# Performance work log

Measured on AMD Instinct MI355X. Metric: run time of the kernel, lower is better.

The kernel has to match this reference:

```python
import jax, jax.numpy as jnp
import numpy as np

EPS = 1e-5
K = 20  # n. neighbors


def _lrelu(x):
    return jnp.where(x >= 0, x, 0.2 * x)


def _bn(x, gamma, beta):
    # training-mode batchnorm over all axes except channel axis 1
    axes = tuple(i for i in range(x.ndim) if i != 1)
    m = jnp.mean(x, axis=axes, keepdims=True)
    v = jnp.var(x, axis=axes, keepdims=True)
    shape = [1, x.shape[1]] + [1] * (x.ndim - 2)
    return (x - m) * jax.lax.rsqrt(v + EPS) * gamma.reshape(shape) + beta.reshape(shape)


def _knn(x, k):
    # x: (B, C, N) -> idx (B, N, k) of nearest neighbors (largest negative sq dist)
    xx = jnp.sum(x * x, axis=1)                      # (B, N)
    inner = jnp.einsum('bcn,bcm->bnm', x, x)          # (B, N, N)
    dist = -xx[:, :, None] + 2.0 * inner - xx[:, None, :]
    _, idx = jax.lax.top_k(dist, k)
    return idx


def _graph_feature(x, k):
    # x: (B, C, N) -> edge features (B, 2C, N, k)
    B = x.shape[0]
    idx = _knn(x, k)                                  # (B, N, k)
    xt = jnp.transpose(x, (0, 2, 1))                  # (B, N, C)
    nbr = xt[jnp.arange(B)[:, None, None], idx]       # (B, N, k, C)
    ctr = xt[:, :, None, :]                           # (B, N, 1, C)
    edge = jnp.concatenate([nbr - ctr, jnp.broadcast_to(ctr, nbr.shape)], axis=-1)
    return jnp.transpose(edge, (0, 3, 1, 2))          # (B, 2C, N, k)


def _conv1d(W, x):
    return jnp.einsum('oc,bcn->bon', W, x)


def _conv2d(W, x):
    return jnp.einsum('oc,bcnk->bonk', W, x)


def setup_inputs() -> dict:
    key = jax.random.key(0)
    ks = jax.random.split(key, 10)
    w = lambda k, s: jax.random.normal(k, s, jnp.float32) * 0.05
    d = {
        'x': jax.random.normal(ks[0], (4, 3, 4096), jnp.float32),
        'W1': w(ks[1], (64, 3)),
        'W2': w(ks[2], (64, 128)),
        'W3': w(ks[3], (64, 128)),
        'W4': w(ks[4], (512, 64)),
        'W5': w(ks[5], (512, 704)),
        'W6': w(ks[6], (256, 512)),
        'W7': w(ks[7], (128, 256)),
        'W8': w(ks[8], (2, 128)),
        'bias8': jnp.zeros((2,), jnp.float32),
    }
    bn_ch = [64, 64, 64, 512, 512, 256, 128]
    for i, c in enumerate(bn_ch, start=1):
        d[f'gamma{i}'] = jnp.ones((c,), jnp.float32)
        d[f'beta{i}'] = jnp.zeros((c,), jnp.float32)
    return d


def reference(x, W1, W2, W3, W4, W5, W6, W7, W8, bias8,
              gamma1, beta1, gamma2, beta2, gamma3, beta3, gamma4, beta4,
              gamma5, beta5, gamma6, beta6, gamma7, beta7):
    N = x.shape[2]
    x1 = _lrelu(_bn(_conv1d(W1, x), gamma1, beta1))                 # (B,64,N)
    e2 = _graph_feature(x1, K)                                      # (B,128,N,k)
    x2 = _lrelu(_bn(_conv2d(W2, e2), gamma2, beta2)).max(axis=-1)   # (B,64,N)
    e3 = _graph_feature(x2, K)
    x3 = _lrelu(_bn(_conv2d(W3, e3), gamma3, beta3)).max(axis=-1)   # (B,64,N)
    x6 = _lrelu(_bn(_conv1d(W4, x3), gamma4, beta4))                # (B,512,N)
    x6 = jnp.broadcast_to(x6.max(axis=-1, keepdims=True), (x6.shape[0], x6.shape[1], N))
    x7 = jnp.concatenate([x1, x2, x3, x6], axis=1)                  # (B,704,N)
    x7 = _lrelu(_bn(_conv1d(W5, x7), gamma5, beta5))
    x7 = _lrelu(_bn(_conv1d(W6, x7), gamma6, beta6))
    x7 = _lrelu(_bn(_conv1d(W7, x7), gamma7, beta7))
    return _conv1d(W8, x7) + bias8[None, :, None]                   # (B,2,N)
```

## Files before the change

### kernel.cpp

```cpp
#include <hip/hip_runtime.h>
#include <math.h>

#define NN 4096
#define BB 4
#define NPT (NN*BB)
#define KK 20
#define EPSB 1e-5f

#define AS_STRIDE 132
#define WS_STRIDE 68
#define SKEW(c) ((((((c)>>2)&7))<<2) + (((c)>>5)*28))

__device__ __forceinline__ float lrelu(float x){ return x >= 0.f ? x : 0.2f*x; }

__global__ void conv1_kernel(const float* __restrict__ x, const float* __restrict__ W1,
                             float* __restrict__ xcat){
  __shared__ float Wl[192];
  int tid = threadIdx.x;
  if (tid < 192) Wl[tid] = W1[tid];
  __syncthreads();
  int p = blockIdx.x*4 + (tid >> 6);
  int o = tid & 63;
  int b = p >> 12, n = p & 4095;
  const float* xb = x + (size_t)b*3*NN + n;
  float acc = Wl[o*3+0]*xb[0] + Wl[o*3+1]*xb[NN] + Wl[o*3+2]*xb[2*NN];
  xcat[(size_t)p*192 + o] = acc;
}

__global__ void stats_pm_kernel(const float* __restrict__ buf, int stride, int ofs,
                                float* __restrict__ psum, float* __restrict__ psumsq, int C){
  int tid = threadIdx.x;
  int lane = tid & 63, g = tid >> 6;
  int o = blockIdx.x*64 + lane;
  int p0 = blockIdx.y*256 + g*64;
  float s = 0.f, ss = 0.f;
  for (int i = 0; i < 64; ++i){
    float v = buf[(size_t)(p0+i)*stride + ofs + o];
    s += v; ss += v*v;
  }
  __shared__ float rs[4][64], rss[4][64];
  rs[g][lane] = s; rss[g][lane] = ss;
  __syncthreads();
  if (g == 0){
    s  = rs[0][lane]+rs[1][lane]+rs[2][lane]+rs[3][lane];
    ss = rss[0][lane]+rss[1][lane]+rss[2][lane]+rss[3][lane];
    psum[(size_t)blockIdx.y*C + o] = s;
    psumsq[(size_t)blockIdx.y*C + o] = ss;
  }
}

__global__ void bn_finalize_kernel(const float* __restrict__ psum, const float* __restrict__ psumsq,
                                   int nparts,
                                   const float* __restrict__ gamma, const float* __restrict__ beta,
                                   float* __restrict__ scale, float* __restrict__ shift,
                                   float invcnt, int C){
  int o = threadIdx.x + blockIdx.x*blockDim.x;
  if (o >= C) return;
  float s = 0.f, ss = 0.f;
  for (int i = 0; i < nparts; ++i){
    s  += psum[(size_t)i*C + o];
    ss += psumsq[(size_t)i*C + o];
  }
  float m = s*invcnt;
  float v = ss*invcnt - m*m;
  v = fmaxf(v, 0.f);
  float sc = gamma[o] * rsqrtf(v + EPSB);
  scale[o] = sc;
  shift[o] = beta[o] - m*sc;
}

__global__ void apply_bn_kernel(float* __restrict__ buf, int stride, int ofs, int log2C,
                                const float* __restrict__ scale, const float* __restrict__ shift){
  int i = blockIdx.x*256 + threadIdx.x;
  int o = i & ((1<<log2C)-1);
  int p = i >> log2C;
  size_t a = (size_t)p*stride + ofs + o;
  float e = buf[a]*scale[o] + shift[o];
  buf[a] = lrelu(e);
}

__global__ void xx_kernel(const float* __restrict__ xcat, int stride, int ofs,
                          float* __restrict__ xx){
  int p = blockIdx.x*256 + threadIdx.x;
  const float4* r = (const float4*)(xcat + (size_t)p*stride + ofs);
  float s = 0.f;
  #pragma unroll
  for (int i = 0; i < 16; ++i){ float4 v = r[i]; s += v.x*v.x + v.y*v.y + v.z*v.z + v.w*v.w; }
  xx[p] = s;
}

__global__ void __launch_bounds__(256, 2)
dist_kernel(const float* __restrict__ xcat, int ofs,
            const float* __restrict__ xx, float* __restrict__ dist, int b){
  __shared__ float As[64*AS_STRIDE + 64];
  __shared__ float Bs[64*AS_STRIDE + 64];
  int tid = threadIdx.x;
  int n0 = blockIdx.x*128, m0 = blockIdx.y*128;
  const float* base = xcat + (size_t)b*NN*192 + ofs;
  int cgrp = (tid & 15)*4;
  float4 vin[8], vw[8];
  #pragma unroll
  for (int j = 0; j < 8; ++j){
    int row = (tid + 256*j) >> 4;
    vin[j] = *(const float4*)(base + (size_t)(n0+row)*192 + cgrp);
    vw[j]  = *(const float4*)(base + (size_t)(m0+row)*192 + cgrp);
  }
  #pragma unroll
  for (int j = 0; j < 8; ++j){
    int row = (tid + 256*j) >> 4, c4 = cgrp;
    float4 v = vin[j];
    As[(c4+0)*AS_STRIDE+SKEW(c4+0)+row]=v.x; As[(c4+1)*AS_STRIDE+SKEW(c4+1)+row]=v.y;
    As[(c4+2)*AS_STRIDE+SKEW(c4+2)+row]=v.z; As[(c4+3)*AS_STRIDE+SKEW(c4+3)+row]=v.w;
    float4 w = vw[j];
    Bs[(c4+0)*AS_STRIDE+SKEW(c4+0)+row]=w.x; Bs[(c4+1)*AS_STRIDE+SKEW(c4+1)+row]=w.y;
    Bs[(c4+2)*AS_STRIDE+SKEW(c4+2)+row]=w.z; Bs[(c4+3)*AS_STRIDE+SKEW(c4+3)+row]=w.w;
  }
  __syncthreads();
  int pA = (tid >> 4)*4, oB = (tid & 15)*4;
  float acc[8][8] = {};
  for (int c = 0; c < 64; ++c){
    const float* arow = &As[c*AS_STRIDE + SKEW(c)];
    const float* brow = &Bs[c*AS_STRIDE + SKEW(c)];
    float4 a0 = *(const float4*)&arow[pA];
    float4 a1 = *(const float4*)&arow[pA + 64];
    float4 b0 = *(const float4*)&brow[oB];
    float4 b1 = *(const float4*)&brow[oB + 64];
    float av[8] = {a0.x,a0.y,a0.z,a0.w,a1.x,a1.y,a1.z,a1.w};
    float bv[8] = {b0.x,b0.y,b0.z,b0.w,b1.x,b1.y,b1.z,b1.w};
    #pragma unroll
    for (int i = 0; i < 8; ++i)
      #pragma unroll
      for (int j = 0; j < 8; ++j)
        acc[i][j] += av[i]*bv[j];
  }
  float xm[8];
  #pragma unroll
  for (int j = 0; j < 4; ++j){
    xm[j]   = xx[b*NN + m0 + oB + j];
    xm[4+j] = xx[b*NN + m0 + 64 + oB + j];
  }
  #pragma unroll
  for (int h = 0; h < 2; ++h){
    #pragma unroll
    for (int i = 0; i < 4; ++i){
      int row = n0 + h*64 + pA + i;
      float xn = xx[b*NN + row];
      int ai = h*4 + i;
      float4 w0, w1;
      w0.x = 2.f*acc[ai][0] - xn - xm[0]; w0.y = 2.f*acc[ai][1] - xn - xm[1];
      w0.z = 2.f*acc[ai][2] - xn - xm[2]; w0.w = 2.f*acc[ai][3] - xn - xm[3];
      w1.x = 2.f*acc[ai][4] - xn - xm[4]; w1.y = 2.f*acc[ai][5] - xn - xm[5];
      w1.z = 2.f*acc[ai][6] - xn - xm[6]; w1.w = 2.f*acc[ai][7] - xn - xm[7];
      float* drow = dist + (size_t)row*NN + m0;
      *(float4*)(drow + oB) = w0;
      *(float4*)(drow + 64 + oB) = w1;
    }
  }
}

__global__ void topk_kernel(const float* __restrict__ dist, int* __restrict__ idxout){
  int n = blockIdx.x;
  int tid = threadIdx.x;
  int wv = tid >> 6;
  const float* row = dist + (size_t)n*NN;
  unsigned k[16];
  #pragma unroll
  for (int i = 0; i < 16; ++i){
    unsigned u = __float_as_uint(row[tid + (i<<8)]);
    k[i] = u ^ (unsigned)(((int)u >> 31) | 0x80000000);
  }
  __shared__ unsigned hist[4][256];
  __shared__ unsigned sufx[257];
  __shared__ unsigned selw[1];
  __shared__ unsigned toff[256];
  __shared__ int mred[4];
  unsigned remaining = KK;
  unsigned prefix = 0;
  #pragma unroll
  for (int lvl = 0; lvl < 4; ++lvl){
    int shift = 24 - lvl*8;
    hist[0][tid]=0; hist[1][tid]=0; hist[2][tid]=0; hist[3][tid]=0;
    __syncthreads();
    unsigned pmask = (lvl == 0) ? 0u : (0xFFFFFFFFu << (shift + 8));
    #pragma unroll
    for (int i = 0; i < 16; ++i){
      if ((k[i] & pmask) == prefix)
        atomicAdd(&hist[wv][(k[i] >> shift) & 255], 1u);
    }
    __syncthreads();
    if (tid < 64){
      unsigned h[4];
      #pragma unroll
      for (int q = 0; q < 4; ++q)
        h[q] = hist[0][tid*4+q]+hist[1][tid*4+q]+hist[2][tid*4+q]+hist[3][tid*4+q];
      unsigned lane_sum = h[0]+h[1]+h[2]+h[3];
      unsigned acc = lane_sum;
      #pragma unroll
      for (int s = 1; s < 64; s <<= 1){
        unsigned o = __shfl_down(acc, s);
        if (tid + s < 64) acc += o;
      }
      unsigned excl = acc - lane_sum;
      sufx[tid*4+3] = excl + h[3];
      sufx[tid*4+2] = excl + h[3] + h[2];
      sufx[tid*4+1] = excl + h[3] + h[2] + h[1];
      sufx[tid*4+0] = excl + h[3] + h[2] + h[1] + h[0];
      if (tid == 0) sufx[256] = 0;
    }
    __syncthreads();
    unsigned s_d = sufx[tid], s_d1 = sufx[tid+1];
    if (s_d >= remaining && s_d1 < remaining) selw[0] = tid;
    __syncthreads();
    unsigned d = selw[0];
    remaining -= sufx[d+1];
    prefix |= d << shift;
  }
  unsigned K20 = prefix;
  unsigned r = remaining;
  unsigned mycount = 0;
  #pragma unroll
  for (int i = 0; i < 16; ++i) if (k[i] > K20) mycount++;
  toff[tid] = mycount;
  __syncthreads();
  if (tid < 64){
    unsigned c0=toff[tid*4], c1=toff[tid*4+1], c2=toff[tid*4+2], c3=toff[tid*4+3];
    unsigned lane_sum = c0+c1+c2+c3;
    unsigned acc = lane_sum;
    #pragma unroll
    for (int s = 1; s < 64; s <<= 1){
      unsigned o = __shfl_up(acc, s);
      if ((int)tid - s >= 0) acc += o;
    }
    unsigned excl = acc - lane_sum;
    sufx[tid*4+0] = excl;
    sufx[tid*4+1] = excl + c0;
    sufx[tid*4+2] = excl + c0 + c1;
    sufx[tid*4+3] = excl + c0 + c1 + c2;
  }
  __syncthreads();
  unsigned pos = sufx[tid];
  int* orow = idxout + n*KK;
  #pragma unroll
  for (int i = 0; i < 16; ++i)
    if (k[i] > K20) orow[pos++] = tid + (i<<8);
  unsigned A = KK - r;
  int last = -1;
  for (unsigned t = 0; t < r; ++t){
    int best = 0x7fffffff;
    #pragma unroll
    for (int i = 0; i < 16; ++i){
      int m = tid + (i<<8);
      if (k[i] == K20 && m > last && m < best) best = m;
    }
    #pragma unroll
    for (int s = 32; s > 0; s >>= 1){
      int o = __shfl_down(best, s);
      best = min(best, o);
    }
    if ((tid & 63) == 0) mred[tid >> 6] = best;
    __syncthreads();
    int w = min(min(mred[0],mred[1]), min(mred[2],mred[3]));
    if (tid == 0) orow[A + t] = w;
    last = w;
    __syncthreads();
  }
}

__global__ void ut_kernel(const float* __restrict__ xcat, int ofs, const float* __restrict__ W,
                          float* __restrict__ U, float* __restrict__ T){
  __shared__ float Wl[64*129];
  int tid = threadIdx.x;
  for (int i = tid; i < 64*128; i += 256){
    int o = i >> 7, c = i & 127;
    Wl[o*129 + c] = W[i];
  }
  __syncthreads();
  int g = tid >> 6, lane = tid & 63;
  int p = blockIdx.x*4 + g;
  float xv = xcat[(size_t)p*192 + ofs + lane];
  const float* wr = Wl + lane*129;
  float u = 0.f, t = 0.f;
  for (int c = 0; c < 64; ++c){
    float xc = __shfl(xv, c);
    float wa = wr[c], wb = wr[64+c];
    u += wa*xc;
    t += (wb - wa)*xc;
  }
  U[(size_t)p*64 + lane] = u;
  T[(size_t)p*64 + lane] = t;
}

__global__ void gather_kernel(const float* __restrict__ U, const float* __restrict__ T,
                              const int* __restrict__ idx,
                              float* __restrict__ psum, float* __restrict__ psumsq,
                              float* __restrict__ vmax, float* __restrict__ vmin){
  int tid = threadIdx.x;
  int g = tid >> 6, lane = tid & 63;
  int p0 = blockIdx.x*64 + g*16;
  float s = 0.f, ss = 0.f;
  for (int pi = 0; pi < 16; ++pi){
    int p = p0 + pi;
    int base = (p >> 12) << 12;
    float t = T[(size_t)p*64 + lane];
    const int* ir = idx + (size_t)p*KK;
    float mx = -INFINITY, mn = INFINITY;
    for (int k = 0; k < KK; ++k){
      int j = ir[k];
      float v = U[(size_t)(base + j)*64 + lane] + t;
      s += v; ss += v*v;
      mx = fmaxf(mx, v); mn = fminf(mn, v);
    }
    vmax[(size_t)p*64 + lane] = mx;
    vmin[(size_t)p*64 + lane] = mn;
  }
  __shared__ float rs[4][64], rss[4][64];
  rs[g][lane] = s; rss[g][lane] = ss;
  __syncthreads();
  if (g == 0){
    s  = rs[0][lane]+rs[1][lane]+rs[2][lane]+rs[3][lane];
    ss = rss[0][lane]+rss[1][lane]+rss[2][lane]+rss[3][lane];
    psum[(size_t)blockIdx.x*64 + lane] = s;
    psumsq[(size_t)blockIdx.x*64 + lane] = ss;
  }
}

__global__ void gapply_kernel(const float* __restrict__ vmax, const float* __restrict__ vmin,
                              const float* __restrict__ scale, const float* __restrict__ shift,
                              float* __restrict__ xcat, int ofs){
  int i = blockIdx.x*256 + threadIdx.x;
  int p = i >> 6, o = i & 63;
  float s = scale[o];
  float v = (s >= 0.f) ? vmax[i] : vmin[i];
  xcat[(size_t)p*192 + ofs + o] = lrelu(s*v + shift[o]);
}

__global__ void __launch_bounds__(256, 2)
mm_kernel(const float* __restrict__ in, int inStride, int inOfs,
          const float* __restrict__ W, int wStride,
          float* __restrict__ out, int outStride,
          const float* __restrict__ bias, int O, int I,
          const float* __restrict__ bnScale, const float* __restrict__ bnShift){
  __shared__ float As[64*AS_STRIDE + 64];
  __shared__ float Ws[64*WS_STRIDE + 64];
  int tid = threadIdx.x;
  int p0 = blockIdx.x*128, o0 = blockIdx.y*64;
  int psub = (tid >> 4)*8, osub = (tid & 15)*4;
  int cgrp = (tid & 15)*4;
  float acc[8][4] = {};
  for (int cc = 0; cc < I; cc += 64){
    float4 sc4 = make_float4(1.f,1.f,1.f,1.f), sh4 = make_float4(0.f,0.f,0.f,0.f);
    if (bnScale){
      sc4 = *(const float4*)(bnScale + cc + cgrp);
      sh4 = *(const float4*)(bnShift + cc + cgrp);
    }
    float4 vin[8], vw[4];
    #pragma unroll
    for (int j = 0; j < 8; ++j){
      int row = (tid + 256*j) >> 4;
      vin[j] = *(const float4*)(in + (size_t)(p0+row)*inStride + inOfs + cc + cgrp);
    }
    #pragma unroll
    for (int j = 0; j < 4; ++j){
      int row = (tid + 256*j) >> 4;
      vw[j] = *(const float4*)(W + (size_t)(o0+row)*wStride + cc + cgrp);
    }
    #pragma unroll
    for (int j = 0; j < 8; ++j){
      int row = (tid + 256*j) >> 4, c4 = cgrp;
      float4 v = vin[j];
      if (bnScale){
        v.x = lrelu(v.x*sc4.x + sh4.x); v.y = lrelu(v.y*sc4.y + sh4.y);
        v.z = lrelu(v.z*sc4.z + sh4.z); v.w = lrelu(v.w*sc4.w + sh4.w);
      }
      As[(c4+0)*AS_STRIDE+SKEW(c4+0)+row]=v.x; As[(c4+1)*AS_STRIDE+SKEW(c4+1)+row]=v.y;
      As[(c4+2)*AS_STRIDE+SKEW(c4+2)+row]=v.z; As[(c4+3)*AS_STRIDE+SKEW(c4+3)+row]=v.w;
    }
    #pragma unroll
    for (int j = 0; j < 4; ++j){
      int row = (tid + 256*j) >> 4, c4 = cgrp;
      float4 v = vw[j];
      Ws[(c4+0)*WS_STRIDE+SKEW(c4+0)+row]=v.x; Ws[(c4+1)*WS_STRIDE+SKEW(c4+1)+row]=v.y;
      Ws[(c4+2)*WS_STRIDE+SKEW(c4+2)+row]=v.z; Ws[(c4+3)*WS_STRIDE+SKEW(c4+3)+row]=v.w;
    }
    __syncthreads();
    for (int c = 0; c < 64; ++c){
      const float* arow = &As[c*AS_STRIDE + SKEW(c)];
      const float* brow = &Ws[c*WS_STRIDE + SKEW(c)];
      float4 a0 = *(const float4*)&arow[psub];
      float4 a1 = *(const float4*)&arow[psub + 4];
      float4 bb = *(const float4*)&brow[osub];
      float av[8] = {a0.x,a0.y,a0.z,a0.w,a1.x,a1.y,a1.z,a1.w};
      float bv[4] = {bb.x,bb.y,bb.z,bb.w};
      #pragma unroll
      for (int i = 0; i < 8; ++i)
        #pragma unroll
        for (int j = 0; j < 4; ++j)
          acc[i][j] += av[i]*bv[j];
    }
    __syncthreads();
  }
  int bIdx = p0 >> 12;
  float bb0=0.f, bb1=0.f, bb2=0.f, bb3=0.f;
  if (bias){
    bb0 = bias[bIdx*O + o0 + osub + 0];
    bb1 = bias[bIdx*O + o0 + osub + 1];
    bb2 = bias[bIdx*O + o0 + osub + 2];
    bb3 = bias[bIdx*O + o0 + osub + 3];
  }
  #pragma unroll
  for (int i = 0; i < 8; ++i){
    float4 w;
    w.x = acc[i][0]+bb0; w.y = acc[i][1]+bb1; w.z = acc[i][2]+bb2; w.w = acc[i][3]+bb3;
    *(float4*)(out + (size_t)(p0+psub+i)*outStride + o0 + osub) = w;
  }
}

__global__ void __launch_bounds__(256, 2)
mm128_kernel(const float* __restrict__ in, int inStride, int inOfs,
             const float* __restrict__ W, int wStride,
             float* __restrict__ out, int outStride,
             const float* __restrict__ bias, int O, int I,
             const float* __restrict__ bnScale, const float* __restrict__ bnShift){
  __shared__ float As[64*AS_STRIDE + 64];
  __shared__ float Ws[64*AS_STRIDE + 64];
  int tid = threadIdx.x;
  int p0 = blockIdx.x*128, o0 = blockIdx.y*128;
  int pA = (tid >> 4)*4, oB = (tid & 15)*4;
  int cgrp = (tid & 15)*4;
  float acc[8][8] = {};
  for (int cc = 0; cc < I; cc += 64){
    float4 sc4 = make_float4(1.f,1.f,1.f,1.f), sh4 = make_float4(0.f,0.f,0.f,0.f);
    if (bnScale){
      sc4 = *(const float4*)(bnScale + cc + cgrp);
      sh4 = *(const float4*)(bnShift + cc + cgrp);
    }
    float4 vin[8], vw[8];
    #pragma unroll
    for (int j = 0; j < 8; ++j){
      int row = (tid + 256*j) >> 4;
      vin[j] = *(const float4*)(in + (size_t)(p0+row)*inStride + inOfs + cc + cgrp);
      vw[j]  = *(const float4*)(W + (size_t)(o0+row)*wStride + cc + cgrp);
    }
    #pragma unroll
    for (int j = 0; j < 8; ++j){
      int row = (tid + 256*j) >> 4, c4 = cgrp;
      float4 v = vin[j];
      if (bnScale){
        v.x = lrelu(v.x*sc4.x + sh4.x); v.y = lrelu(v.y*sc4.y + sh4.y);
        v.z = lrelu(v.z*sc4.z + sh4.z); v.w = lrelu(v.w*sc4.w + sh4.w);
      }
      As[(c4+0)*AS_STRIDE+SKEW(c4+0)+row]=v.x; As[(c4+1)*AS_STRIDE+SKEW(c4+1)+row]=v.y;
      As[(c4+2)*AS_STRIDE+SKEW(c4+2)+row]=v.z; As[(c4+3)*AS_STRIDE+SKEW(c4+3)+row]=v.w;
      float4 w = vw[j];
      Ws[(c4+0)*AS_STRIDE+SKEW(c4+0)+row]=w.x; Ws[(c4+1)*AS_STRIDE+SKEW(c4+1)+row]=w.y;
      Ws[(c4+2)*AS_STRIDE+SKEW(c4+2)+row]=w.z; Ws[(c4+3)*AS_STRIDE+SKEW(c4+3)+row]=w.w;
    }
    __syncthreads();
    for (int c = 0; c < 64; ++c){
      const float* arow = &As[c*AS_STRIDE + SKEW(c)];
      const float* brow = &Ws[c*AS_STRIDE + SKEW(c)];
      float4 a0 = *(const float4*)&arow[pA];
      float4 a1 = *(const float4*)&arow[pA + 64];
      float4 b0 = *(const float4*)&brow[oB];
      float4 b1 = *(const float4*)&brow[oB + 64];
      float av[8] = {a0.x,a0.y,a0.z,a0.w,a1.x,a1.y,a1.z,a1.w};
      float bv[8] = {b0.x,b0.y,b0.z,b0.w,b1.x,b1.y,b1.z,b1.w};
      #pragma unroll
      for (int i = 0; i < 8; ++i)
        #pragma unroll
        for (int j = 0; j < 8; ++j)
          acc[i][j] += av[i]*bv[j];
    }
    __syncthreads();
  }
  int bIdx = p0 >> 12;
  float bb[8] = {0.f,0.f,0.f,0.f,0.f,0.f,0.f,0.f};
  if (bias){
    #pragma unroll
    for (int j = 0; j < 4; ++j){
      bb[j]   = bias[bIdx*O + o0 + oB + j];
      bb[4+j] = bias[bIdx*O + o0 + 64 + oB + j];
    }
  }
  #pragma unroll
  for (int h = 0; h < 2; ++h){
    #pragma unroll
    for (int i = 0; i < 4; ++i){
      int row = p0 + h*64 + pA + i;
      int ai = h*4 + i;
      float4 w0, w1;
      w0.x = acc[ai][0]+bb[0]; w0.y = acc[ai][1]+bb[1];
      w0.z = acc[ai][2]+bb[2]; w0.w = acc[ai][3]+bb[3];
      w1.x = acc[ai][4]+bb[4]; w1.y = acc[ai][5]+bb[5];
      w1.z = acc[ai][6]+bb[6]; w1.w = acc[ai][7]+bb[7];
      float* orow = out + (size_t)row*outStride + o0;
      *(float4*)(orow + oB) = w0;
      *(float4*)(orow + 64 + oB) = w1;
    }
  }
}

__global__ void __launch_bounds__(256, 2)
conv4stats_kernel(const float* __restrict__ xcat, const float* __restrict__ W4,
                  float* __restrict__ psum, float* __restrict__ psumsq,
                  float* __restrict__ pmax, float* __restrict__ pmin){
  __shared__ float As[64*AS_STRIDE + 64];
  __shared__ float Ws[64*AS_STRIDE + 64];
  int tid = threadIdx.x;
  int p0 = blockIdx.x*128, o0 = blockIdx.y*128;
  int pA = (tid >> 4)*4, oB = (tid & 15)*4;
  int cgrp = (tid & 15)*4;
  float4 vin[8], vw[8];
  #pragma unroll
  for (int j = 0; j < 8; ++j){
    int row = (tid + 256*j) >> 4;
    vin[j] = *(const float4*)(xcat + (size_t)(p0+row)*192 + 128 + cgrp);
    vw[j]  = *(const float4*)(W4 + (size_t)(o0+row)*64 + cgrp);
  }
  #pragma unroll
  for (int j = 0; j < 8; ++j){
    int row = (tid + 256*j) >> 4, c4 = cgrp;
    float4 v = vin[j];
    As[(c4+0)*AS_STRIDE+SKEW(c4+0)+row]=v.x; As[(c4+1)*AS_STRIDE+SKEW(c4+1)+row]=v.y;
    As[(c4+2)*AS_STRIDE+SKEW(c4+2)+row]=v.z; As[(c4+3)*AS_STRIDE+SKEW(c4+3)+row]=v.w;
    float4 w = vw[j];
    Ws[(c4+0)*AS_STRIDE+SKEW(c4+0)+row]=w.x; Ws[(c4+1)*AS_STRIDE+SKEW(c4+1)+row]=w.y;
    Ws[(c4+2)*AS_STRIDE+SKEW(c4+2)+row]=w.z; Ws[(c4+3)*AS_STRIDE+SKEW(c4+3)+row]=w.w;
  }
  __syncthreads();
  float acc[8][8] = {};
  for (int c = 0; c < 64; ++c){
    const float* arow = &As[c*AS_STRIDE + SKEW(c)];
    const float* brow = &Ws[c*AS_STRIDE + SKEW(c)];
    float4 a0 = *(const float4*)&arow[pA];
    float4 a1 = *(const float4*)&arow[pA + 64];
    float4 b0 = *(const float4*)&brow[oB];
    float4 b1 = *(const float4*)&brow[oB + 64];
    float av[8] = {a0.x,a0.y,a0.z,a0.w,a1.x,a1.y,a1.z,a1.w};
    float bv[8] = {b0.x,b0.y,b0.z,b0.w,b1.x,b1.y,b1.z,b1.w};
    #pragma unroll
    for (int i = 0; i < 8; ++i)
      #pragma unroll
      for (int j = 0; j < 8; ++j)
        acc[i][j] += av[i]*bv[j];
  }
  float cs[8], cq[8], cmx[8], cmn[8];
  #pragma unroll
  for (int j = 0; j < 8; ++j){
    float s = 0.f, q = 0.f, mx = -INFINITY, mn = INFINITY;
    #pragma unroll
    for (int i = 0; i < 8; ++i){
      float v = acc[i][j];
      s += v; q += v*v; mx = fmaxf(mx, v); mn = fminf(mn, v);
    }
    cs[j]=s; cq[j]=q; cmx[j]=mx; cmn[j]=mn;
  }
  __syncthreads();
  int r = tid >> 4;
  #pragma unroll
  for (int j = 0; j < 8; ++j){
    int col = (j < 4) ? (oB + j) : (64 + oB + (j-4));
    As[r*128 + col]        = cs[j];
    As[2048 + r*128 + col] = cq[j];
    Ws[r*128 + col]        = cmx[j];
    Ws[2048 + r*128 + col] = cmn[j];
  }
  __syncthreads();
  if (tid < 128){
    float ts = 0.f, tq = 0.f, tm = -INFINITY, tn = INFINITY;
    for (int rr = 0; rr < 16; ++rr){
      ts += As[rr*128 + tid];
      tq += As[2048 + rr*128 + tid];
      tm = fmaxf(tm, Ws[rr*128 + tid]);
      tn = fminf(tn, Ws[2048 + rr*128 + tid]);
    }
    size_t slot = (size_t)blockIdx.x*512 + o0 + tid;
    psum[slot] = ts; psumsq[slot] = tq; pmax[slot] = tm; pmin[slot] = tn;
  }
}

__global__ void x6v_kernel(const float* __restrict__ pmax, const float* __restrict__ pmin,
                           const float* __restrict__ scale, const float* __restrict__ shift,
                           float* __restrict__ x6v){
  int t = blockIdx.x*256 + threadIdx.x;
  int b = t >> 9, o = t & 511;
  float mx = -INFINITY, mn = INFINITY;
  for (int pt = b*32; pt < b*32+32; ++pt){
    mx = fmaxf(mx, pmax[(size_t)pt*512 + o]);
    mn = fminf(mn, pmin[(size_t)pt*512 + o]);
  }
  float s = scale[o];
  float v = (s >= 0.f) ? mx : mn;
  x6v[t] = lrelu(s*v + shift[o]);
}

__global__ void bias5_kernel(const float* __restrict__ W5, const float* __restrict__ x6v,
                             float* __restrict__ b5){
  __shared__ float xl[512];
  int tid = threadIdx.x;
  int t = blockIdx.x*256 + tid;
  int b = t >> 9, o = t & 511;
  for (int i = tid; i < 512; i += 256) xl[i] = x6v[(b<<9) + i];
  __syncthreads();
  const float* wr = W5 + (size_t)o*704 + 192;
  float acc = 0.f;
  for (int c = 0; c < 512; ++c) acc += wr[c]*xl[c];
  b5[t] = acc;
}

__global__ void conv8_kernel(const float* __restrict__ r7, const float* __restrict__ W8,
                             const float* __restrict__ bias8,
                             const float* __restrict__ scale, const float* __restrict__ shift,
                             float* __restrict__ out){
  __shared__ float Wl[256];
  __shared__ float scl[128], shl[128];
  int tid = threadIdx.x;
  Wl[tid] = W8[tid];
  if (tid < 128){ scl[tid] = scale[tid]; shl[tid] = shift[tid]; }
  __syncthreads();
  int p = blockIdx.x*256 + tid;
  int b = p >> 12, n = p & 4095;
  const float4* row = (const float4*)(r7 + (size_t)p*128);
  float a0 = 0.f, a1 = 0.f;
  #pragma unroll
  for (int i = 0; i < 32; ++i){
    float4 v = row[i];
    v.x = lrelu(v.x*scl[i*4+0] + shl[i*4+0]);
    v.y = lrelu(v.y*scl[i*4+1] + shl[i*4+1]);
    v.z = lrelu(v.z*scl[i*4+2] + shl[i*4+2]);
    v.w = lrelu(v.w*scl[i*4+3] + shl[i*4+3]);
    a0 += v.x*Wl[i*4] + v.y*Wl[i*4+1] + v.z*Wl[i*4+2] + v.w*Wl[i*4+3];
    a1 += v.x*Wl[128+i*4] + v.y*Wl[128+i*4+1] + v.z*Wl[128+i*4+2] + v.w*Wl[128+i*4+3];
  }
  out[(size_t)(b*2+0)*NN + n] = a0 + bias8[0];
  out[(size_t)(b*2+1)*NN + n] = a1 + bias8[1];
}

extern "C" void kernel_launch(void* const* d_in, const int* in_sizes, int n_in,
                              void* d_out, int out_size, void* d_ws, size_t ws_size,
                              hipStream_t stream){
  const float* x     = (const float*)d_in[0];
  const float* W1    = (const float*)d_in[1];
  const float* W2    = (const float*)d_in[2];
  const float* W3    = (const float*)d_in[3];
  const float* W4    = (const float*)d_in[4];
  const float* W5    = (const float*)d_in[5];
  const float* W6    = (const float*)d_in[6];
  const float* W7    = (const float*)d_in[7];
  const float* W8    = (const float*)d_in[8];
  const float* bias8 = (const float*)d_in[9];
  const float* gamma[8]; const float* beta[8];
  for (int i = 1; i <= 7; ++i){
    gamma[i] = (const float*)d_in[10 + 2*(i-1)];
    beta[i]  = (const float*)d_in[11 + 2*(i-1)];
  }
  float* out = (float*)d_out;

  float* ws = (float*)d_ws;
  size_t off = 0;
  float* xcat  = ws + off; off += (size_t)NPT*192;
  float* U     = ws + off; off += (size_t)NPT*64;
  float* T     = ws + off; off += (size_t)NPT*64;
  float* xx    = ws + off; off += NPT;
  int*   idx   = (int*)(ws + off); off += (size_t)NPT*KK;
  float* psum  = ws + off; off += 128*512;
  float* psumsq= ws + off; off += 128*512;
  float* pmax  = ws + off; off += 128*512;
  float* pmin  = ws + off; off += 128*512;
  float* scale = ws + off; off += 512;
  float* shift = ws + off; off += 512;
  float* x6v   = ws + off; off += 2048;
  float* b5    = ws + off; off += 2048;
  float* big   = ws + off;
  float* dist  = big;
  float* vmaxB = big;
  float* vminB = big + (size_t)NPT*64;
  float* r5    = big;
  float* r6    = big + (size_t)NPT*512;
  float* r7    = big + (size_t)NPT*512 + (size_t)NPT*256;

  conv1_kernel<<<NPT/4, 256, 0, stream>>>(x, W1, xcat);
  stats_pm_kernel<<<dim3(1,64), 256, 0, stream>>>(xcat, 192, 0, psum, psumsq, 64);
  bn_finalize_kernel<<<1, 64, 0, stream>>>(psum, psumsq, 64, gamma[1], beta[1], scale, shift, 1.f/16384.f, 64);
  apply_bn_kernel<<<NPT*64/256, 256, 0, stream>>>(xcat, 192, 0, 6, scale, shift);

  xx_kernel<<<NPT/256, 256, 0, stream>>>(xcat, 192, 0, xx);
  for (int b = 0; b < BB; ++b){
    dist_kernel<<<dim3(32,32), 256, 0, stream>>>(xcat, 0, xx, dist, b);
    topk_kernel<<<NN, 256, 0, stream>>>(dist, idx + (size_t)b*NN*KK);
  }

  ut_kernel<<<NPT/4, 256, 0, stream>>>(xcat, 0, W2, U, T);
  gather_kernel<<<256, 256, 0, stream>>>(U, T, idx, psum, psumsq, vmaxB, vminB);
  bn_finalize_kernel<<<1, 64, 0, stream>>>(psum, psumsq, 256, gamma[2], beta[2], scale, shift, 1.f/327680.f, 64);
  gapply_kernel<<<NPT*64/256, 256, 0, stream>>>(vmaxB, vminB, scale, shift, xcat, 64);

  xx_kernel<<<NPT/256, 256, 0, stream>>>(xcat, 192, 64, xx);
  for (int b = 0; b < BB; ++b){
    dist_kernel<<<dim3(32,32), 256, 0, stream>>>(xcat, 64, xx, dist, b);
    topk_kernel<<<NN, 256, 0, stream>>>(dist, idx + (size_t)b*NN*KK);
  }

  ut_kernel<<<NPT/4, 256, 0, stream>>>(xcat, 64, W3, U, T);
  gather_kernel<<<256, 256, 0, stream>>>(U, T, idx, psum, psumsq, vmaxB, vminB);
  bn_finalize_kernel<<<1, 64, 0, stream>>>(psum, psumsq, 256, gamma[3], beta[3], scale, shift, 1.f/327680.f, 64);
  gapply_kernel<<<NPT*64/256, 256, 0, stream>>>(vmaxB, vminB, scale, shift, xcat, 128);

  conv4stats_kernel<<<dim3(NPT/128, 4), 256, 0, stream>>>(xcat, W4, psum, psumsq, pmax, pmin);
  bn_finalize_kernel<<<1, 512, 0, stream>>>(psum, psumsq, 128, gamma[4], beta[4], scale, shift, 1.f/16384.f, 512);
  x6v_kernel<<<8, 256, 0, stream>>>(pmax, pmin, scale, shift, x6v);
  bias5_kernel<<<8, 256, 0, stream>>>(W5, x6v, b5);

  mm128_kernel<<<dim3(NPT/128, 4), 256, 0, stream>>>(xcat, 192, 0, W5, 704, r5, 512, b5, 512, 192, nullptr, nullptr);
  stats_pm_kernel<<<dim3(8,64), 256, 0, stream>>>(r5, 512, 0, psum, psumsq, 512);
  bn_finalize_kernel<<<1, 512, 0, stream>>>(psum, psumsq, 64, gamma[5], beta[5], scale, shift, 1.f/16384.f, 512);

  mm128_kernel<<<dim3(NPT/128, 2), 256, 0, stream>>>(r5, 512, 0, W6, 512, r6, 256, nullptr, 256, 512, scale, shift);
  stats_pm_kernel<<<dim3(4,64), 256, 0, stream>>>(r6, 256, 0, psum, psumsq, 256);
  bn_finalize_kernel<<<1, 256, 0, stream>>>(psum, psumsq, 64, gamma[6], beta[6], scale, shift, 1.f/16384.f, 256);

  mm_kernel<<<dim3(NPT/128, 2), 256, 0, stream>>>(r6, 256, 0, W7, 256, r7, 128, nullptr, 128, 256, scale, shift);
  stats_pm_kernel<<<dim3(2,64), 256, 0, stream>>>(r7, 128, 0, psum, psumsq, 128);
  bn_finalize_kernel<<<1, 128, 0, stream>>>(psum, psumsq, 64, gamma[7], beta[7], scale, shift, 1.f/16384.f, 128);

  conv8_kernel<<<NPT/256, 256, 0, stream>>>(r7, W8, bias8, scale, shift, out);
}
```

Baseline: 1.335 ms.

## Exploit distance symmetry and halve K-tile depth to raise GEMM occupancy

```diff
diff --git a/kernel.cpp b/kernel.cpp
--- a/kernel.cpp
+++ b/kernel.cpp
@@ -89,71 +89,101 @@
   xx[p] = s;
 }
 
-__global__ void __launch_bounds__(256, 2)
+__global__ void __launch_bounds__(256, 4)
 dist_kernel(const float* __restrict__ xcat, int ofs,
             const float* __restrict__ xx, float* __restrict__ dist, int b){
-  __shared__ float As[64*AS_STRIDE + 64];
-  __shared__ float Bs[64*AS_STRIDE + 64];
-  int tid = threadIdx.x;
-  int n0 = blockIdx.x*128, m0 = blockIdx.y*128;
+  int bx = blockIdx.x, by = blockIdx.y;
+  if (by > bx) return;
+  __shared__ float As[32*AS_STRIDE + 64];
+  __shared__ float Bs[32*AS_STRIDE + 64];
+  int tid = threadIdx.x;
+  int n0 = by*128, m0 = bx*128;
   const float* base = xcat + (size_t)b*NN*192 + ofs;
-  int cgrp = (tid & 15)*4;
-  float4 vin[8], vw[8];
-  #pragma unroll
-  for (int j = 0; j < 8; ++j){
-    int row = (tid + 256*j) >> 4;
-    vin[j] = *(const float4*)(base + (size_t)(n0+row)*192 + cgrp);
-    vw[j]  = *(const float4*)(base + (size_t)(m0+row)*192 + cgrp);
-  }
-  #pragma unroll
-  for (int j = 0; j < 8; ++j){
-    int row = (tid + 256*j) >> 4, c4 = cgrp;
-    float4 v = vin[j];
-    As[(c4+0)*AS_STRIDE+SKEW(c4+0)+row]=v.x; As[(c4+1)*AS_STRIDE+SKEW(c4+1)+row]=v.y;
-    As[(c4+2)*AS_STRIDE+SKEW(c4+2)+row]=v.z; As[(c4+3)*AS_STRIDE+SKEW(c4+3)+row]=v.w;
-    float4 w = vw[j];
-    Bs[(c4+0)*AS_STRIDE+SKEW(c4+0)+row]=w.x; Bs[(c4+1)*AS_STRIDE+SKEW(c4+1)+row]=w.y;
-    Bs[(c4+2)*AS_STRIDE+SKEW(c4+2)+row]=w.z; Bs[(c4+3)*AS_STRIDE+SKEW(c4+3)+row]=w.w;
-  }
-  __syncthreads();
   int pA = (tid >> 4)*4, oB = (tid & 15)*4;
+  int cgrp = (tid & 7)*4;
   float acc[8][8] = {};
-  for (int c = 0; c < 64; ++c){
-    const float* arow = &As[c*AS_STRIDE + SKEW(c)];
-    const float* brow = &Bs[c*AS_STRIDE + SKEW(c)];
-    float4 a0 = *(const float4*)&arow[pA];
-    float4 a1 = *(const float4*)&arow[pA + 64];
-    float4 b0 = *(const float4*)&brow[oB];
-    float4 b1 = *(const float4*)&brow[oB + 64];
-    float av[8] = {a0.x,a0.y,a0.z,a0.w,a1.x,a1.y,a1.z,a1.w};
-    float bv[8] = {b0.x,b0.y,b0.z,b0.w,b1.x,b1.y,b1.z,b1.w};
-    #pragma unroll
-    for (int i = 0; i < 8; ++i)
+  for (int h = 0; h < 2; ++h){
+    int cb = h*32;
+    float4 vin[4], vw[4];
+    #pragma unroll
+    for (int j = 0; j < 4; ++j){
+      int row = (tid + 256*j) >> 3;
+      vin[j] = *(const float4*)(base + (size_t)(n0+row)*192 + cb + cgrp);
+      vw[j]  = *(const float4*)(base + (size_t)(m0+row)*192 + cb + cgrp);
+    }
+    if (h) __syncthreads();
+    #pragma unroll
+    for (int j = 0; j < 4; ++j){
+      int row = (tid + 256*j) >> 3, c4 = cgrp;
+      float4 v = vin[j];
+      As[(c4+0)*AS_STRIDE+SKEW(c4+0)+row]=v.x; As[(c4+1)*AS_STRIDE+SKEW(c4+1)+row]=v.y;
+      As[(c4+2)*AS_STRIDE+SKEW(c4+2)+row]=v.z; As[(c4+3)*AS_STRIDE+SKEW(c4+3)+row]=v.w;
+      float4 w = vw[j];
+      Bs[(c4+0)*AS_STRIDE+SKEW(c4+0)+row]=w.x; Bs[(c4+1)*AS_STRIDE+SKEW(c4+1)+row]=w.y;
+      Bs[(c4+2)*AS_STRIDE+SKEW(c4+2)+row]=w.z; Bs[(c4+3)*AS_STRIDE+SKEW(c4+3)+row]=w.w;
+    }
+    __syncthreads();
+    for (int c = 0; c < 32; ++c){
+      const float* arow = &As[c*AS_STRIDE + SKEW(c)];
+      const float* brow = &Bs[c*AS_STRIDE + SKEW(c)];
+      float4 a0 = *(const float4*)&arow[pA];
+      float4 a1 = *(const float4*)&arow[pA + 64];
+      float4 b0 = *(const float4*)&brow[oB];
+      float4 b1 = *(const float4*)&brow[oB + 64];
+      float av[8] = {a0.x,a0.y,a0.z,a0.w,a1.x,a1.y,a1.z,a1.w};
+      float bv[8] = {b0.x,b0.y,b0.z,b0.w,b1.x,b1.y,b1.z,b1.w};
       #pragma unroll
-      for (int j = 0; j < 8; ++j)
-        acc[i][j] += av[i]*bv[j];
-  }
-  float xm[8];
+      for (int i = 0; i < 8; ++i)
+        #pragma unroll
+        for (int j = 0; j < 8; ++j)
+          acc[i][j] += av[i]*bv[j];
+    }
+  }
+  float xmv[8], xnv[8];
   #pragma unroll
   for (int j = 0; j < 4; ++j){
-    xm[j]   = xx[b*NN + m0 + oB + j];
-    xm[4+j] = xx[b*NN + m0 + 64 + oB + j];
-  }
-  #pragma unroll
-  for (int h = 0; h < 2; ++h){
+    xmv[j]   = xx[b*NN + m0 + oB + j];
+    xmv[4+j] = xx[b*NN + m0 + 64 + oB + j];
+    xnv[j]   = xx[b*NN + n0 + pA + j];
+    xnv[4+j] = xx[b*NN + n0 + 64 + pA + j];
+  }
+  #pragma unroll
+  for (int hh = 0; hh < 2; ++hh){
     #pragma unroll
     for (int i = 0; i < 4; ++i){
-      int row = n0 + h*64 + pA + i;
-      float xn = xx[b*NN + row];
-      int ai = h*4 + i;
+      int row = n0 + hh*64 + pA + i;
+      float xn = xnv[hh*4 + i];
+      int ai = hh*4 + i;
       float4 w0, w1;
-      w0.x = 2.f*acc[ai][0] - xn - xm[0]; w0.y = 2.f*acc[ai][1] - xn - xm[1];
-      w0.z = 2.f*acc[ai][2] - xn - xm[2]; w0.w = 2.f*acc[ai][3] - xn - xm[3];
-      w1.x = 2.f*acc[ai][4] - xn - xm[4]; w1.y = 2.f*acc[ai][5] - xn - xm[5];
-      w1.z = 2.f*acc[ai][6] - xn - xm[6]; w1.w = 2.f*acc[ai][7] - xn - xm[7];
+      w0.x = 2.f*acc[ai][0] - xn - xmv[0]; w0.y = 2.f*acc[ai][1] - xn - xmv[1];
+      w0.z = 2.f*acc[ai][2] - xn - xmv[2]; w0.w = 2.f*acc[ai][3] - xn - xmv[3];
+      w1.x = 2.f*acc[ai][4] - xn - xmv[4]; w1.y = 2.f*acc[ai][5] - xn - xmv[5];
+      w1.z = 2.f*acc[ai][6] - xn - xmv[6]; w1.w = 2.f*acc[ai][7] - xn - xmv[7];
       float* drow = dist + (size_t)row*NN + m0;
       *(float4*)(drow + oB) = w0;
       *(float4*)(drow + 64 + oB) = w1;
+    }
+  }
+  if (bx != by){
+    #pragma unroll
+    for (int jh = 0; jh < 2; ++jh){
+      #pragma unroll
+      for (int jj = 0; jj < 4; ++jj){
+        int j = jh*4 + jj;
+        float xm = xmv[j];
+        float4 lo, hi;
+        lo.x = 2.f*acc[0][j] - xm - xnv[0];
+        lo.y = 2.f*acc[1][j] - xm - xnv[1];
+        lo.z = 2.f*acc[2][j] - xm - xnv[2];
+        lo.w = 2.f*acc[3][j] - xm - xnv[3];
+        hi.x = 2.f*acc[4][j] - xm - xnv[4];
+        hi.y = 2.f*acc[5][j] - xm - xnv[5];
+        hi.z = 2.f*acc[6][j] - xm - xnv[6];
+        hi.w = 2.f*acc[7][j] - xm - xnv[7];
+        float* drow = dist + (size_t)(m0 + jh*64 + oB + jj)*NN + n0;
+        *(float4*)(drow + pA) = lo;
+        *(float4*)(drow + 64 + pA) = hi;
+      }
     }
   }
 }
@@ -334,39 +364,40 @@
   xcat[(size_t)p*192 + ofs + o] = lrelu(s*v + shift[o]);
 }
 
-__global__ void __launch_bounds__(256, 2)
+__global__ void __launch_bounds__(256, 4)
 mm_kernel(const float* __restrict__ in, int inStride, int inOfs,
           const float* __restrict__ W, int wStride,
           float* __restrict__ out, int outStride,
           const float* __restrict__ bias, int O, int I,
           const float* __restrict__ bnScale, const float* __restrict__ bnShift){
-  __shared__ float As[64*AS_STRIDE + 64];
-  __shared__ float Ws[64*WS_STRIDE + 64];
+  __shared__ float As[32*AS_STRIDE + 64];
+  __shared__ float Ws[32*WS_STRIDE + 64];
   int tid = threadIdx.x;
   int p0 = blockIdx.x*128, o0 = blockIdx.y*64;
   int psub = (tid >> 4)*8, osub = (tid & 15)*4;
-  int cgrp = (tid & 15)*4;
+  int cgrp = (tid & 7)*4;
   float acc[8][4] = {};
-  for (int cc = 0; cc < I; cc += 64){
+  for (int cc = 0; cc < I; cc += 32){
     float4 sc4 = make_float4(1.f,1.f,1.f,1.f), sh4 = make_float4(0.f,0.f,0.f,0.f);
     if (bnScale){
       sc4 = *(const float4*)(bnScale + cc + cgrp);
       sh4 = *(const float4*)(bnShift + cc + cgrp);
     }
-    float4 vin[8], vw[4];
-    #pragma unroll
-    for (int j = 0; j < 8; ++j){
-      int row = (tid + 256*j) >> 4;
+    float4 vin[4], vw[2];
+    #pragma unroll
+    for (int j = 0; j < 4; ++j){
+      int row = (tid + 256*j) >> 3;
       vin[j] = *(const float4*)(in + (size_t)(p0+row)*inStride + inOfs + cc + cgrp);
     }
     #pragma unroll
-    for (int j = 0; j < 4; ++j){
-      int row = (tid + 256*j) >> 4;
+    for (int j = 0; j < 2; ++j){
+      int row = (tid + 256*j) >> 3;
       vw[j] = *(const float4*)(W + (size_t)(o0+row)*wStride + cc + cgrp);
     }
-    #pragma unroll
-    for (int j = 0; j < 8; ++j){
-      int row = (tid + 256*j) >> 4, c4 = cgrp;
+    if (cc) __syncthreads();
+    #pragma unroll
+    for (int j = 0; j < 4; ++j){
+      int row = (tid + 256*j) >> 3, c4 = cgrp;
       float4 v = vin[j];
       if (bnScale){
         v.x = lrelu(v.x*sc4.x + sh4.x); v.y = lrelu(v.y*sc4.y + sh4.y);
@@ -376,14 +407,14 @@
       As[(c4+2)*AS_STRIDE+SKEW(c4+2)+row]=v.z; As[(c4+3)*AS_STRIDE+SKEW(c4+3)+row]=v.w;
     }
     #pragma unroll
-    for (int j = 0; j < 4; ++j){
-      int row = (tid + 256*j) >> 4, c4 = cgrp;
+    for (int j = 0; j < 2; ++j){
+      int row = (tid + 256*j) >> 3, c4 = cgrp;
       float4 v = vw[j];
       Ws[(c4+0)*WS_STRIDE+SKEW(c4+0)+row]=v.x; Ws[(c4+1)*WS_STRIDE+SKEW(c4+1)+row]=v.y;
       Ws[(c4+2)*WS_STRIDE+SKEW(c4+2)+row]=v.z; Ws[(c4+3)*WS_STRIDE+SKEW(c4+3)+row]=v.w;
     }
     __syncthreads();
-    for (int c = 0; c < 64; ++c){
+    for (int c = 0; c < 32; ++c){
       const float* arow = &As[c*AS_STRIDE + SKEW(c)];
       const float* brow = &Ws[c*WS_STRIDE + SKEW(c)];
       float4 a0 = *(const float4*)&arow[psub];
@@ -397,7 +428,6 @@
         for (int j = 0; j < 4; ++j)
           acc[i][j] += av[i]*bv[j];
     }
-    __syncthreads();
   }
   int bIdx = p0 >> 12;
   float bb0=0.f, bb1=0.f, bb2=0.f, bb3=0.f;
@@ -415,35 +445,36 @@
   }
 }
 
-__global__ void __launch_bounds__(256, 2)
+__global__ void __launch_bounds__(256, 4)
 mm128_kernel(const float* __restrict__ in, int inStride, int inOfs,
              const float* __restrict__ W, int wStride,
              float* __restrict__ out, int outStride,
              const float* __restrict__ bias, int O, int I,
              const float* __restrict__ bnScale, const float* __restrict__ bnShift){
-  __shared__ float As[64*AS_STRIDE + 64];
-  __shared__ float Ws[64*AS_STRIDE + 64];
+  __shared__ float As[32*AS_STRIDE + 64];
+  __shared__ float Ws[32*AS_STRIDE + 64];
   int tid = threadIdx.x;
   int p0 = blockIdx.x*128, o0 = blockIdx.y*128;
   int pA = (tid >> 4)*4, oB = (tid & 15)*4;
-  int cgrp = (tid & 15)*4;
+  int cgrp = (tid & 7)*4;
   float acc[8][8] = {};
-  for (int cc = 0; cc < I; cc += 64){
+  for (int cc = 0; cc < I; cc += 32){
     float4 sc4 = make_float4(1.f,1.f,1.f,1.f), sh4 = make_float4(0.f,0.f,0.f,0.f);
     if (bnScale){
       sc4 = *(const float4*)(bnScale + cc + cgrp);
       sh4 = *(const float4*)(bnShift + cc + cgrp);
     }
-    float4 vin[8], vw[8];
-    #pragma unroll
-    for (int j = 0; j < 8; ++j){
-      int row = (tid + 256*j) >> 4;
+    float4 vin[4], vw[4];
+    #pragma unroll
+    for (int j = 0; j < 4; ++j){
+      int row = (tid + 256*j) >> 3;
       vin[j] = *(const float4*)(in + (size_t)(p0+row)*inStride + inOfs + cc + cgrp);
       vw[j]  = *(const float4*)(W + (size_t)(o0+row)*wStride + cc + cgrp);
     }
-    #pragma unroll
-    for (int j = 0; j < 8; ++j){
-      int row = (tid + 256*j) >> 4, c4 = cgrp;
+    if (cc) __syncthreads();
+    #pragma unroll
+    for (int j = 0; j < 4; ++j){
+      int row = (tid + 256*j) >> 3, c4 = cgrp;
       float4 v = vin[j];
       if (bnScale){
         v.x = lrelu(v.x*sc4.x + sh4.x); v.y = lrelu(v.y*sc4.y + sh4.y);
@@ -456,7 +487,7 @@
       Ws[(c4+2)*AS_STRIDE+SKEW(c4+2)+row]=w.z; Ws[(c4+3)*AS_STRIDE+SKEW(c4+3)+row]=w.w;
     }
     __syncthreads();
-    for (int c = 0; c < 64; ++c){
+    for (int c = 0; c < 32; ++c){
       const float* arow = &As[c*AS_STRIDE + SKEW(c)];
       const float* brow = &Ws[c*AS_STRIDE + SKEW(c)];
       float4 a0 = *(const float4*)&arow[pA];
@@ -471,7 +502,6 @@
         for (int j = 0; j < 8; ++j)
           acc[i][j] += av[i]*bv[j];
     }
-    __syncthreads();
   }
   int bIdx = p0 >> 12;
   float bb[8] = {0.f,0.f,0.f,0.f,0.f,0.f,0.f,0.f};
@@ -500,49 +530,53 @@
   }
 }
 
-__global__ void __launch_bounds__(256, 2)
+__global__ void __launch_bounds__(256, 3)
 conv4stats_kernel(const float* __restrict__ xcat, const float* __restrict__ W4,
                   float* __restrict__ psum, float* __restrict__ psumsq,
                   float* __restrict__ pmax, float* __restrict__ pmin){
-  __shared__ float As[64*AS_STRIDE + 64];
-  __shared__ float Ws[64*AS_STRIDE + 64];
+  __shared__ float As[32*AS_STRIDE + 64];
+  __shared__ float Ws[32*AS_STRIDE + 64];
   int tid = threadIdx.x;
   int p0 = blockIdx.x*128, o0 = blockIdx.y*128;
   int pA = (tid >> 4)*4, oB = (tid & 15)*4;
-  int cgrp = (tid & 15)*4;
-  float4 vin[8], vw[8];
-  #pragma unroll
-  for (int j = 0; j < 8; ++j){
-    int row = (tid + 256*j) >> 4;
-    vin[j] = *(const float4*)(xcat + (size_t)(p0+row)*192 + 128 + cgrp);
-    vw[j]  = *(const float4*)(W4 + (size_t)(o0+row)*64 + cgrp);
-  }
-  #pragma unroll
-  for (int j = 0; j < 8; ++j){
-    int row = (tid + 256*j) >> 4, c4 = cgrp;
-    float4 v = vin[j];
-    As[(c4+0)*AS_STRIDE+SKEW(c4+0)+row]=v.x; As[(c4+1)*AS_STRIDE+SKEW(c4+1)+row]=v.y;
-    As[(c4+2)*AS_STRIDE+SKEW(c4+2)+row]=v.z; As[(c4+3)*AS_STRIDE+SKEW(c4+3)+row]=v.w;
-    float4 w = vw[j];
-    Ws[(c4+0)*AS_STRIDE+SKEW(c4+0)+row]=w.x; Ws[(c4+1)*AS_STRIDE+SKEW(c4+1)+row]=w.y;
-    Ws[(c4+2)*AS_STRIDE+SKEW(c4+2)+row]=w.z; Ws[(c4+3)*AS_STRIDE+SKEW(c4+3)+row]=w.w;
-  }
-  __syncthreads();
+  int cgrp = (tid & 7)*4;
   float acc[8][8] = {};
-  for (int c = 0; c < 64; ++c){
-    const float* arow = &As[c*AS_STRIDE + SKEW(c)];
-    const float* brow = &Ws[c*AS_STRIDE + SKEW(c)];
-    float4 a0 = *(const float4*)&arow[pA];
-    float4 a1 = *(const float4*)&arow[pA + 64];
-    float4 b0 = *(const float4*)&brow[oB];
-    float4 b1 = *(const float4*)&brow[oB + 64];
-    float av[8] = {a0.x,a0.y,a0.z,a0.w,a1.x,a1.y,a1.z,a1.w};
-    float bv[8] = {b0.x,b0.y,b0.z,b0.w,b1.x,b1.y,b1.z,b1.w};
-    #pragma unroll
-    for (int i = 0; i < 8; ++i)
+  for (int h = 0; h < 2; ++h){
+    int cb = h*32;
+    float4 vin[4], vw[4];
+    #pragma unroll
+    for (int j = 0; j < 4; ++j){
+      int row = (tid + 256*j) >> 3;
+      vin[j] = *(const float4*)(xcat + (size_t)(p0+row)*192 + 128 + cb + cgrp);
+      vw[j]  = *(const float4*)(W4 + (size_t)(o0+row)*64 + cb + cgrp);
+    }
+    if (h) __syncthreads();
+    #pragma unroll
+    for (int j = 0; j < 4; ++j){
+      int row = (tid + 256*j) >> 3, c4 = cgrp;
+      float4 v = vin[j];
+      As[(c4+0)*AS_STRIDE+SKEW(c4+0)+row]=v.x; As[(c4+1)*AS_STRIDE+SKEW(c4+1)+row]=v.y;
+      As[(c4+2)*AS_STRIDE+SKEW(c4+2)+row]=v.z; As[(c4+3)*AS_STRIDE+SKEW(c4+3)+row]=v.w;
+      float4 w = vw[j];
+      Ws[(c4+0)*AS_STRIDE+SKEW(c4+0)+row]=w.x; Ws[(c4+1)*AS_STRIDE+SKEW(c4+1)+row]=w.y;
+      Ws[(c4+2)*AS_STRIDE+SKEW(c4+2)+row]=w.z; Ws[(c4+3)*AS_STRIDE+SKEW(c4+3)+row]=w.w;
+    }
+    __syncthreads();
+    for (int c = 0; c < 32; ++c){
+      const float* arow = &As[c*AS_STRIDE + SKEW(c)];
+      const float* brow = &Ws[c*AS_STRIDE + SKEW(c)];
+      float4 a0 = *(const float4*)&arow[pA];
+      float4 a1 = *(const float4*)&arow[pA + 64];
+      float4 b0 = *(const float4*)&brow[oB];
+      float4 b1 = *(const float4*)&brow[oB + 64];
+      float av[8] = {a0.x,a0.y,a0.z,a0.w,a1.x,a1.y,a1.z,a1.w};
+      float bv[8] = {b0.x,b0.y,b0.z,b0.w,b1.x,b1.y,b1.z,b1.w};
       #pragma unroll
-      for (int j = 0; j < 8; ++j)
-        acc[i][j] += av[i]*bv[j];
+      for (int i = 0; i < 8; ++i)
+        #pragma unroll
+        for (int j = 0; j < 8; ++j)
+          acc[i][j] += av[i]*bv[j];
+    }
   }
   float cs[8], cq[8], cmx[8], cmn[8];
   #pragma unroll
```

Measured after the change: 1.394 ms. 1.04x slower.
